# Kernel optimization log

Measured on AMD Instinct MI355X. Metric: run time of the kernel, lower is better.

## Reference

```python
import jax, jax.numpy as jnp
import numpy as np

NG = 1024      # graphs
NPG = 128      # nodes per graph (forced by lin1 = Linear(128*hid, 128))
N = NG * NPG   # 131072 nodes
DEG = 16       # avg in-graph degree
E = N * DEG    # 2,097,152 edges
IN, H = 4, 64


def setup_inputs() -> dict:
    key = jax.random.key(0)
    ks = jax.random.split(key, 24)
    x = jax.random.normal(ks[0], (N, IN), jnp.float32)
    # edges constrained within each 128-node graph
    src = jax.random.randint(ks[1], (E,), 0, NPG)
    dst = jax.random.randint(ks[2], (E,), 0, NPG)
    off = jnp.repeat(jnp.arange(NG, dtype=jnp.int32) * NPG, NPG * DEG)
    edge_index = jnp.stack([src.astype(jnp.int32) + off, dst.astype(jnp.int32) + off])
    g = lambda k, shp, fan: jax.random.normal(k, shp, jnp.float32) / np.float32(np.sqrt(fan))
    return {
        "x": x, "edge_index": edge_index,
        # GATv2Conv(4->64)
        "Wl": g(ks[3], (IN, H), IN), "bl": jnp.zeros((H,), jnp.float32),
        "Wr": g(ks[4], (IN, H), IN), "br": jnp.zeros((H,), jnp.float32),
        "att_v2": g(ks[5], (H,), H), "b_v2": jnp.zeros((H,), jnp.float32),
        # GATConv #1 (64->64)
        "Wg1": g(ks[6], (H, H), H), "as1": g(ks[7], (H,), H),
        "ad1": g(ks[8], (H,), H), "bg1": jnp.zeros((H,), jnp.float32),
        # GATConv #2 (64->64)
        "Wg2": g(ks[9], (H, H), H), "as2": g(ks[10], (H,), H),
        "ad2": g(ks[11], (H,), H), "bg2": jnp.zeros((H,), jnp.float32),
        # LayerNorm(64)
        "ln_g": jnp.ones((H,), jnp.float32), "ln_b": jnp.zeros((H,), jnp.float32),
        # heads: Linear(128*64 -> 128), Linear(128 -> 1)
        "W1": g(ks[12], (NPG * H, 128), NPG * H), "b1": jnp.zeros((128,), jnp.float32),
        "W2": g(ks[13], (128, 1), 128), "b2": jnp.zeros((1,), jnp.float32),
    }


def _seg_softmax(logits, seg):
    # stable softmax over edges grouped by destination node
    m = jax.ops.segment_max(logits, seg, num_segments=N)
    ex = jnp.exp(logits - m[seg])
    s = jax.ops.segment_sum(ex, seg, num_segments=N)
    return ex / (s[seg] + 1e-16)


def _gatv2(x, src, dst, Wl, bl, Wr, br, att, bias):
    xl = x @ Wl + bl                       # source transform [N,H]
    xr = x @ Wr + br                       # target transform [N,H]
    e = jax.nn.leaky_relu(xl[src] + xr[dst], 0.2) @ att   # [E]
    a = _seg_softmax(e, dst)
    out = jax.ops.segment_sum(a[:, None] * xl[src], dst, num_segments=N)
    return out + bias


def _gat(x, src, dst, W, a_src, a_dst, bias):
    # GATConv default: add self-loops
    loop = jnp.arange(N, dtype=src.dtype)
    s2 = jnp.concatenate([src, loop]); d2 = jnp.concatenate([dst, loop])
    xw = x @ W                             # [N,H]
    al_s = xw @ a_src; al_d = xw @ a_dst   # per-node attention halves [N]
    e = jax.nn.leaky_relu(al_s[s2] + al_d[d2], 0.2)
    a = _seg_softmax(e, d2)
    out = jax.ops.segment_sum(a[:, None] * xw[s2], d2, num_segments=N)
    return out + bias


def _layernorm(x, g, b, eps=1e-5):
    mu = jnp.mean(x, -1, keepdims=True)
    var = jnp.mean(jnp.square(x - mu), -1, keepdims=True)
    return (x - mu) * jax.lax.rsqrt(var + eps) * g + b


def reference(x, edge_index, Wl, bl, Wr, br, att_v2, b_v2,
              Wg1, as1, ad1, bg1, Wg2, as2, ad2, bg2,
              ln_g, ln_b, W1, b1, W2, b2):
    src, dst = edge_index[0], edge_index[1]
    h = jax.nn.leaky_relu(_gatv2(x, src, dst, Wl, bl, Wr, br, att_v2, b_v2), 0.01)
    h = _layernorm(h, ln_g, ln_b)
    h = jax.nn.relu(_gat(h, src, dst, Wg1, as1, ad1, bg1))
    h = jax.nn.relu(_gat(h, src, dst, Wg2, as2, ad2, bg2))
    # linearize: batch is sorted with exactly NPG nodes per graph -> reshape
    h = h.reshape(NG, NPG * H)
    h = jax.nn.leaky_relu(h @ W1 + b1, 0.01)
    return jax.nn.sigmoid(h @ W2 + b2)     # [NG, 1]
```

## Files before the change

kernel.cpp:

```cpp
#include <hip/hip_runtime.h>
#include <hip/hip_bf16.h>

#define NGRAPH 1024
#define NPG 128
#define EPG 2048
#define ETOT (NGRAPH*NPG*16)
#define HD 64

typedef unsigned int uint;
typedef unsigned short ushort_t;
typedef __attribute__((ext_vector_type(8))) short s8v;
typedef __attribute__((ext_vector_type(4))) float f32x4;

#define MFMA16 __builtin_amdgcn_mfma_f32_16x16x32_bf16

__device__ __forceinline__ float lrelu(float x, float s){ return fmaxf(x, x*s); }
__device__ __forceinline__ float b2lo(uint u){ return __uint_as_float(u << 16); }
__device__ __forceinline__ float b2hi(uint u){ return __uint_as_float(u & 0xFFFF0000u); }
__device__ __forceinline__ uint pkbf(float a, float b){
  union { __hip_bfloat162 h; uint u; } t;
  t.h = __hip_bfloat162{__float2bfloat16(a), __float2bfloat16(b)};
  return t.u;
}
__device__ __forceinline__ ushort_t bfb(float v){
  union { __hip_bfloat16 h; ushort_t u; } t; t.h = __float2bfloat16(v); return t.u;
}
union U4S8 { uint4 u; s8v s; };
__device__ __forceinline__ s8v bcs8(uint4 u){ U4S8 t; t.u = u; return t.s; }
__device__ __forceinline__ s8v pk8(uint4 x, uint4 y){
  U4S8 t;
  t.u.x = pkbf(__uint_as_float(x.x), __uint_as_float(x.y));
  t.u.y = pkbf(__uint_as_float(x.z), __uint_as_float(x.w));
  t.u.z = pkbf(__uint_as_float(y.x), __uint_as_float(y.y));
  t.u.w = pkbf(__uint_as_float(y.z), __uint_as_float(y.w));
  return t.s;
}
#define DPP_ADD(v, ctrl) ((v) + __int_as_float(__builtin_amdgcn_update_dpp(0, __float_as_int(v), (ctrl), 0xF, 0xF, false)))

__device__ __forceinline__ int oswz(int r, int p){ return (r<<5) | ((((p>>2) ^ (r & 7))<<2) | (p & 3)); }
__device__ __forceinline__ int obase(int r, int oc){ return (r<<5) | (((oc) ^ (r & 7))<<2); }
__device__ __forceinline__ int t64(int r, int p){ return (r<<6) | ((((p>>2) ^ (r & 15))<<2) | (p & 3)); }
__device__ __forceinline__ int t64b(int r, int q){ return (r<<6) | (((q ^ (r & 15))<<2)); }
__device__ __forceinline__ int fP16(int r, int k){ return (r<<7) | (((((k>>2) ^ r) & 31)<<2) | (k & 3)); }
__device__ __forceinline__ int fP16b(int r, int q){ return (r<<7) | ((((q ^ r) & 31))<<2); }

#define O_H   0
#define O_T   4096
#define O_P   8192
#define O_E   10240
#define O_SOF 12288
#define O_ALS 12353
#define O_ALD 12481
#define SM_SZ 12609

__device__ __forceinline__ void aggregate_rounds(
    uint* SM, const ushort_t* soff16, const float* eva, const ushort_t* edsG,
    const float* selfw, const float* biasp, bool dorelu,
    int tid, int wv, int lw, int lq)
{
  float* Pf = (float*)(SM + O_P);
  ushort_t* sH16 = (ushort_t*)(SM + O_H);
  float bj = biasp[16*wv + lw];
  for (int q = 0; q < 8; q++) {
    uint4 z = {0,0,0,0};
    *(uint4*)&SM[O_P + tid*8]     = z;
    *(uint4*)&SM[O_P + tid*8 + 4] = z;
    __syncthreads();
    int p0 = soff16[q*16], p1 = soff16[q*16 + 16];
    for (int p = p0 + tid; p < p1; p += 256) {
      int sd = edsG[p];
      atomicAdd(&Pf[fP16((sd >> 8) - q*16, sd & 127)], eva[p]);
    }
    if (selfw && tid < 16)
      atomicAdd(&Pf[fP16(tid, q*16 + tid)], selfw[q*16 + tid]);
    __syncthreads();
    f32x4 c = {0.f,0.f,0.f,0.f};
    #pragma unroll
    for (int ks = 0; ks < 4; ks++) {
      int kk = ks*32 + lq*8;
      uint4 f0 = *(uint4*)&Pf[fP16b(lw, (kk>>2))];
      uint4 f1 = *(uint4*)&Pf[fP16b(lw, (kk>>2)+1)];
      s8v a = pk8(f0, f1);
      s8v b = bcs8(*(uint4*)&SM[O_T + t64b(16*wv + lw, kk>>3)]);
      c = MFMA16(a, b, c, 0, 0, 0);
    }
    int col = 16*wv + lw;
    #pragma unroll
    for (int rg = 0; rg < 4; rg++) {
      float v = c[rg] + bj;
      v = dorelu ? fmaxf(v, 0.f) : lrelu(v, 0.01f);
      int r = q*16 + lq*4 + rg;
      sH16[oswz(r, col>>1)*2 + (col&1)] = bfb(v);
    }
    __syncthreads();
  }
}

__global__ __launch_bounds__(256, 3) void gnn_fused(
    const float* __restrict__ x, const int* __restrict__ ei,
    const float* __restrict__ Wl, const float* __restrict__ bl,
    const float* __restrict__ Wr, const float* __restrict__ br,
    const float* __restrict__ att, const float* __restrict__ bv2,
    const float* __restrict__ Wg1, const float* __restrict__ as1,
    const float* __restrict__ ad1, const float* __restrict__ bg1,
    const float* __restrict__ Wg2, const float* __restrict__ as2,
    const float* __restrict__ ad2, const float* __restrict__ bg2,
    const float* __restrict__ lng, const float* __restrict__ lnb,
    uint* __restrict__ hout, uint* __restrict__ edsd_ws)
{
  __shared__ uint SM[SM_SZ];
  float*    eva   = (float*)(SM + O_E);
  ushort_t* soff16= (ushort_t*)(SM + O_SOF);
  float*    als   = (float*)(SM + O_ALS);
  float*    ald   = (float*)(SM + O_ALD);
  ushort_t* sH16  = (ushort_t*)(SM + O_H);
  ushort_t* sT16  = (ushort_t*)(SM + O_T);

  const int g    = blockIdx.x;
  const int tid  = threadIdx.x;
  const int lane = tid & 63;
  const int wv   = tid >> 6;
  const int lw   = lane & 15;
  const int lq   = lane >> 4;
  const int oc   = lane & 7;
  const int ebase = g * EPG;
  uint* eg = edsd_ws + (size_t)g * 1024;
  const ushort_t* edsG = (const ushort_t*)eg;

  {
    int* spos = (int*)(SM + O_P + 1024);
    ushort_t* edsL = (ushort_t*)(SM + O_P);
    if (tid < NPG) spos[tid] = 0;
    __syncthreads();
    for (int e = tid; e < EPG; e += 256)
      atomicAdd(&spos[ei[ETOT + ebase + e] - g*NPG], 1);
    __syncthreads();
    if (wv == 0) {
      int c0 = spos[lane], c1 = spos[lane + 64];
      #pragma unroll
      for (int o = 1; o < 64; o <<= 1) { int t = __shfl_up(c0, o); if (lane >= o) c0 += t; }
      #pragma unroll
      for (int o = 1; o < 64; o <<= 1) { int t = __shfl_up(c1, o); if (lane >= o) c1 += t; }
      int tot0 = __shfl(c0, 63);
      soff16[lane + 1]  = (ushort_t)c0;
      soff16[lane + 65] = (ushort_t)(c1 + tot0);
      if (lane == 0) soff16[0] = 0;
    }
    __syncthreads();
    if (tid < NPG) spos[tid] = soff16[tid];
    __syncthreads();
    for (int e = tid; e < EPG; e += 256) {
      int s = ei[ebase + e] - g*NPG;
      int d = ei[ETOT + ebase + e] - g*NPG;
      int p = atomicAdd(&spos[d], 1);
      edsL[p] = (ushort_t)(s | (d << 8));
    }
    __syncthreads();
  }

  {
    #pragma unroll
    for (int i = 0; i < 4; i++) eg[tid + i*256] = SM[O_P + tid + i*256];

    const int pl = lane & 31, hb = lane >> 5;
    const float2 wl0 = *(const float2*)&Wl[0*64 + 2*pl];
    const float2 wl1 = *(const float2*)&Wl[1*64 + 2*pl];
    const float2 wl2 = *(const float2*)&Wl[2*64 + 2*pl];
    const float2 wl3 = *(const float2*)&Wl[3*64 + 2*pl];
    const float2 wr0 = *(const float2*)&Wr[0*64 + 2*pl];
    const float2 wr1 = *(const float2*)&Wr[1*64 + 2*pl];
    const float2 wr2 = *(const float2*)&Wr[2*64 + 2*pl];
    const float2 wr3 = *(const float2*)&Wr[3*64 + 2*pl];
    const float2 blp = *(const float2*)&bl[2*pl];
    const float2 brp = *(const float2*)&br[2*pl];
    const float4* x4 = (const float4*)x + (size_t)g * NPG;
    for (int st = 0; st < 16; st++) {
      int i = st*8 + wv*2 + hb;
      float4 xi = x4[i];
      float l0 = blp.x + xi.x*wl0.x + xi.y*wl1.x + xi.z*wl2.x + xi.w*wl3.x;
      float l1 = blp.y + xi.x*wl0.y + xi.y*wl1.y + xi.z*wl2.y + xi.w*wl3.y;
      float r0 = brp.x + xi.x*wr0.x + xi.y*wr1.x + xi.z*wr2.x + xi.w*wr3.x;
      float r1 = brp.y + xi.x*wr0.y + xi.y*wr1.y + xi.z*wr2.y + xi.w*wr3.y;
      SM[O_H + oswz(i, pl)] = pkbf(l0, l1);
      SM[O_T + oswz(i, pl)] = pkbf(r0, r1);
    }
  }
  __syncthreads();

  {
    const int grp = lane >> 3;
    const ushort_t* edsL = (const ushort_t*)(SM + O_P);
    float4 atA = *(const float4*)&att[oc*8];
    float4 atB = *(const float4*)&att[oc*8 + 4];
    int base = wv * 512;
    for (int stp = 0; stp < 64; stp++) {
      int e  = base + stp*8 + grp;
      int sd = edsL[e];
      int s  = sd & 127, d = sd >> 8;
      uint4 ql = *(uint4*)&SM[O_H + obase(s, oc)];
      uint4 qr = *(uint4*)&SM[O_T + obase(d, oc)];
      float acc, v;
      v = b2lo(ql.x)+b2lo(qr.x); acc  = lrelu(v,0.2f)*atA.x;
      v = b2hi(ql.x)+b2hi(qr.x); acc += lrelu(v,0.2f)*atA.y;
      v = b2lo(ql.y)+b2lo(qr.y); acc += lrelu(v,0.2f)*atA.z;
      v = b2hi(ql.y)+b2hi(qr.y); acc += lrelu(v,0.2f)*atA.w;
      v = b2lo(ql.z)+b2lo(qr.z); acc += lrelu(v,0.2f)*atB.x;
      v = b2hi(ql.z)+b2hi(qr.z); acc += lrelu(v,0.2f)*atB.y;
      v = b2lo(ql.w)+b2lo(qr.w); acc += lrelu(v,0.2f)*atB.z;
      v = b2hi(ql.w)+b2hi(qr.w); acc += lrelu(v,0.2f)*atB.w;
      acc = DPP_ADD(acc, 0x111); acc = DPP_ADD(acc, 0x112); acc = DPP_ADD(acc, 0x114);
      if ((lane & 7) == 7) eva[e] = acc;
    }
  }
  __syncthreads();

  {
    const int g16 = tid >> 4, sl = tid & 15;
    for (int it = 0; it < 8; it++) {
      int d = it*16 + g16;
      int p0 = soff16[d], p1 = soff16[d+1];
      float m = -1e30f;
      for (int p = p0 + sl; p < p1; p += 16) m = fmaxf(m, eva[p]);
      #pragma unroll
      for (int o = 1; o < 16; o <<= 1) m = fmaxf(m, __shfl_xor(m, o));
      float ssum = 0.f;
      for (int p = p0 + sl; p < p1; p += 16) { float ex = __expf(eva[p]-m); ssum += ex; eva[p] = ex; }
      #pragma unroll
      for (int o = 1; o < 16; o <<= 1) ssum += __shfl_xor(ssum, o);
      float rnm = 1.f / (ssum + 1e-16f);
      for (int p = p0 + sl; p < p1; p += 16) eva[p] *= rnm;
    }
    ushort_t* xl16 = (ushort_t*)(SM + O_H);
    int j = tid & 63, spb = tid >> 6;
    for (int i = 0; i < 16; i++) {
      int sp = spb*16 + i;
      float v0 = __uint_as_float((uint)xl16[oswz(2*sp,   j>>1)*2 + (j&1)] << 16);
      float v1 = __uint_as_float((uint)xl16[oswz(2*sp+1, j>>1)*2 + (j&1)] << 16);
      SM[O_T + t64(j, sp)] = pkbf(v0, v1);
    }
  }
  __syncthreads();

  aggregate_rounds(SM, soff16, eva, edsG, nullptr, bv2, false, tid, wv, lw, lq);

  {
    int pl = lane & 31, hb = lane >> 5;
    float2 gv = *(const float2*)&lng[2*pl];
    float2 bv = *(const float2*)&lnb[2*pl];
    for (int it = 0; it < 16; it++) {
      int d = it*8 + wv*2 + hb;
      uint w = SM[O_H + oswz(d, pl)];
      float v0 = b2lo(w), v1 = b2hi(w);
      float s1 = v0 + v1, s2 = v0*v0 + v1*v1;
      #pragma unroll
      for (int o = 1; o < 32; o <<= 1) { s1 += __shfl_xor(s1, o); s2 += __shfl_xor(s2, o); }
      float mu  = s1 * 0.015625f;
      float var = s2 * 0.015625f - mu*mu;
      float rs  = rsqrtf(var + 1e-5f);
      SM[O_H + oswz(d, pl)] = pkbf((v0-mu)*rs*gv.x + bv.x, (v1-mu)*rs*gv.y + bv.y);
    }
  }
  __syncthreads();

  for (int layer = 0; layer < 2; layer++) {
    const float* Wg  = layer ? Wg2 : Wg1;
    const float* avs = layer ? as2 : as1;
    const float* avd = layer ? ad2 : ad1;
    const float* bg  = layer ? bg2 : bg1;
    float* was = (float*)(SM + O_P);
    float* wad = was + 64;
    ushort_t* wg16 = (ushort_t*)(SM + O_E);

    if (tid < 128) {
      const float* av = (tid < 64) ? avs : avd;
      float* dst = (tid < 64) ? was : wad;
      int k = tid & 63;
      float acc = 0.f;
      #pragma unroll
      for (int jj = 0; jj < 16; jj++) {
        float4 w = *(const float4*)&Wg[k*64 + jj*4];
        float4 a = *(const float4*)&av[jj*4];
        acc += w.x*a.x + w.y*a.y + w.z*a.z + w.w*a.w;
      }
      dst[k] = acc;
    } else {
      int t2 = tid - 128;
      #pragma unroll
      for (int i = 0; i < 8; i++) {
        int idx = t2 + i*128;
        int k = idx >> 4, j4 = (idx & 15)*4;
        float4 w = *(const float4*)&Wg[k*64 + j4];
        wg16[oswz(j4+0, k>>1)*2 + (k&1)] = bfb(w.x);
        wg16[oswz(j4+1, k>>1)*2 + (k&1)] = bfb(w.y);
        wg16[oswz(j4+2, k>>1)*2 + (k&1)] = bfb(w.z);
        wg16[oswz(j4+3, k>>1)*2 + (k&1)] = bfb(w.w);
      }
    }
    __syncthreads();

    {
      int row = 16*wv + lw;
      s8v a0 = bcs8(*(uint4*)&SM[O_E + obase(row, lq)]);
      s8v a1 = bcs8(*(uint4*)&SM[O_E + obase(row, 4+lq)]);
      #pragma unroll
      for (int nt = 0; nt < 8; nt++) {
        int d = nt*16 + lw;
        s8v b0 = bcs8(*(uint4*)&SM[O_H + obase(d, lq)]);
        s8v b1 = bcs8(*(uint4*)&SM[O_H + obase(d, 4+lq)]);
        f32x4 c = {0.f,0.f,0.f,0.f};
        c = MFMA16(a0, b0, c, 0, 0, 0);
        c = MFMA16(a1, b1, c, 0, 0, 0);
        int j0 = 16*wv + lq*4;
        #pragma unroll
        for (int rg = 0; rg < 4; rg++)
          sT16[t64(j0+rg, d>>1)*2 + (d&1)] = bfb(c[rg]);
      }
    }
    __syncthreads();

    {
      float4 ws0 = *(float4*)&was[oc*8], ws1 = *(float4*)&was[oc*8 + 4];
      float4 wd0 = *(float4*)&wad[oc*8], wd1 = *(float4*)&wad[oc*8 + 4];
      for (int ps = 0; ps < 4; ps++) {
        int n = ps*32 + (tid >> 3);
        uint4 q = *(uint4*)&SM[O_H + obase(n, oc)];
        float f0=b2lo(q.x), f1=b2hi(q.x), f2=b2lo(q.y), f3=b2hi(q.y);
        float f4=b2lo(q.z), f5=b2hi(q.z), f6=b2lo(q.w), f7=b2hi(q.w);
        float sa = f0*ws0.x+f1*ws0.y+f2*ws0.z+f3*ws0.w+f4*ws1.x+f5*ws1.y+f6*ws1.z+f7*ws1.w;
        float sd = f0*wd0.x+f1*wd0.y+f2*wd0.z+f3*wd0.w+f4*wd1.x+f5*wd1.y+f6*wd1.z+f7*wd1.w;
        sa = DPP_ADD(sa, 0x111); sa = DPP_ADD(sa, 0x112); sa = DPP_ADD(sa, 0x114);
        sd = DPP_ADD(sd, 0x111); sd = DPP_ADD(sd, 0x112); sd = DPP_ADD(sd, 0x114);
        if ((lane & 7) == 7) { als[n] = sa; ald[n] = sd; }
      }
    }
    __syncthreads();

    #pragma unroll
    for (int i = 0; i < 4; i++) {
      uint w = eg[tid + i*256];
      int e = (tid + i*256)*2;
      int sd0 = w & 0xFFFF, sd1 = w >> 16;
      eva[e]   = lrelu(als[sd0 & 127] + ald[sd0 >> 8], 0.2f);
      eva[e+1] = lrelu(als[sd1 & 127] + ald[sd1 >> 8], 0.2f);
    }
    __syncthreads();

    {
      const int g16 = tid >> 4, sl = tid & 15;
      for (int it = 0; it < 8; it++) {
        int d = it*16 + g16;
        int p0 = soff16[d], p1 = soff16[d+1];
        float se = lrelu(als[d] + ald[d], 0.2f);
        float m = se;
        for (int p = p0 + sl; p < p1; p += 16) m = fmaxf(m, eva[p]);
        #pragma unroll
        for (int o = 1; o < 16; o <<= 1) m = fmaxf(m, __shfl_xor(m, o));
        float ex0 = __expf(se - m);
        float ssum = 0.f;
        for (int p = p0 + sl; p < p1; p += 16) { float ex = __expf(eva[p]-m); ssum += ex; eva[p] = ex; }
        #pragma unroll
        for (int o = 1; o < 16; o <<= 1) ssum += __shfl_xor(ssum, o);
        float rnm = 1.f / (ssum + ex0 + 1e-16f);
        for (int p = p0 + sl; p < p1; p += 16) eva[p] *= rnm;
        if (sl == 0) als[d] = ex0 * rnm;
      }
    }
    __syncthreads();

    aggregate_rounds(SM, soff16, eva, edsG, als, bg, true, tid, wv, lw, lq);
  }

  {
    uint* hg = hout + (size_t)g * 4096;
    #pragma unroll
    for (int i = 0; i < 16; i++) {
      int idx = tid + i*256;
      hg[idx] = SM[O_H + oswz(idx >> 5, idx & 31)];
    }
  }
}

__global__ __launch_bounds__(256) void w1_transpose(const float* __restrict__ W1,
                                                    uint* __restrict__ w1t)
{
  __shared__ float sw[64*130];
  const int tid = threadIdx.x;
  const int k0 = blockIdx.x * 64;
  #pragma unroll
  for (int i = 0; i < 8; i++) {
    int idx = tid + i*256;
    int r = idx >> 5, c4 = (idx & 31)*4;
    *(float4*)&sw[r*130 + c4] = *(const float4*)&W1[(size_t)(k0+r)*128 + c4];
  }
  __syncthreads();
  #pragma unroll
  for (int i = 0; i < 16; i++) {
    int idx = tid + i*256;
    int c = idx >> 5, kp = idx & 31;
    w1t[(size_t)c*4096 + (k0>>1) + kp] = pkbf(sw[(2*kp)*130 + c], sw[(2*kp+1)*130 + c]);
  }
}

__global__ __launch_bounds__(256) void head_gemm(
    const uint* __restrict__ hbuf, const uint* __restrict__ w1t,
    float* __restrict__ partial)
{
  __shared__ uint sAh[2048];
  __shared__ uint sBh[4096];
  const int tid = threadIdx.x, lane = tid & 63, wv = tid >> 6;
  const int lw = lane & 15, lq = lane >> 4;
  const int g0 = blockIdx.x * 64;
  const int ks = blockIdx.y;
  f32x4 acc[8];
  #pragma unroll
  for (int i = 0; i < 8; i++) acc[i] = f32x4{0.f,0.f,0.f,0.f};

  for (int ch = 0; ch < 8; ch++) {
    int pb = ks*256 + ch*32;
    #pragma unroll
    for (int i = 0; i < 2; i++) {
      int idx = tid + i*256; int r = idx >> 3, q4 = idx & 7;
      uint4 v = *(const uint4*)&hbuf[(size_t)(g0+r)*4096 + pb + q4*4];
      *(uint4*)&sAh[(r<<5) | ((q4 ^ (r & 7))<<2)] = v;
    }
    #pragma unroll
    for (int i = 0; i < 4; i++) {
      int idx = tid + i*256; int r = idx >> 3, q4 = idx & 7;
      uint4 v = *(const uint4*)&w1t[(size_t)r*4096 + pb + q4*4];
      *(uint4*)&sBh[(r<<5) | ((q4 ^ (r & 7))<<2)] = v;
    }
    __syncthreads();
    int ra = 16*wv + lw;
    s8v a0 = bcs8(*(uint4*)&sAh[obase(ra, lq)]);
    s8v a1 = bcs8(*(uint4*)&sAh[obase(ra, 4+lq)]);
    #pragma unroll
    for (int nt = 0; nt < 8; nt++) {
      int c = nt*16 + lw;
      s8v b0 = bcs8(*(uint4*)&sBh[obase(c, lq)]);
      s8v b1 = bcs8(*(uint4*)&sBh[obase(c, 4+lq)]);
      acc[nt] = MFMA16(a0, b0, acc[nt], 0, 0, 0);
      acc[nt] = MFMA16(a1, b1, acc[nt], 0, 0, 0);
    }
    __syncthreads();
  }
  float* pp = partial + (size_t)ks*131072;
  #pragma unroll
  for (int nt = 0; nt < 8; nt++) {
    int c = nt*16 + lw;
    int r0 = g0 + 16*wv + lq*4;
    #pragma unroll
    for (int rg = 0; rg < 4; rg++)
      pp[(size_t)(r0+rg)*128 + c] = acc[nt][rg];
  }
}

__global__ __launch_bounds__(64) void head_out(
    const float* __restrict__ partial, const float* __restrict__ b1,
    const float* __restrict__ W2, const float* __restrict__ b2,
    float* __restrict__ out)
{
  const int g = blockIdx.x;
  const int l = threadIdx.x;
  float v0 = b1[l], v1 = b1[64 + l];
  #pragma unroll
  for (int s = 0; s < 16; s++) {
    v0 += partial[(size_t)s*131072 + g*128 + l];
    v1 += partial[(size_t)s*131072 + g*128 + 64 + l];
  }
  float sum = lrelu(v0, 0.01f)*W2[l] + lrelu(v1, 0.01f)*W2[64 + l];
  #pragma unroll
  for (int m = 32; m > 0; m >>= 1) sum += __shfl_xor(sum, m);
  if (l == 0) out[g] = 1.f / (1.f + __expf(-(sum + b2[0])));
}

extern "C" void kernel_launch(void* const* d_in, const int* in_sizes, int n_in,
                              void* d_out, int out_size, void* d_ws, size_t ws_size,
                              hipStream_t stream) {
  const float* x   = (const float*)d_in[0];
  const int*   ei  = (const int*)  d_in[1];
  const float* Wl  = (const float*)d_in[2];
  const float* bl_ = (const float*)d_in[3];
  const float* Wr  = (const float*)d_in[4];
  const float* br_ = (const float*)d_in[5];
  const float* att = (const float*)d_in[6];
  const float* bv2 = (const float*)d_in[7];
  const float* Wg1 = (const float*)d_in[8];
  const float* as1 = (const float*)d_in[9];
  const float* ad1 = (const float*)d_in[10];
  const float* bg1 = (const float*)d_in[11];
  const float* Wg2 = (const float*)d_in[12];
  const float* as2 = (const float*)d_in[13];
  const float* ad2 = (const float*)d_in[14];
  const float* bg2 = (const float*)d_in[15];
  const float* lng = (const float*)d_in[16];
  const float* lnb = (const float*)d_in[17];
  const float* W1  = (const float*)d_in[18];
  const float* b1  = (const float*)d_in[19];
  const float* W2  = (const float*)d_in[20];
  const float* b2  = (const float*)d_in[21];
  float* out = (float*)d_out;

  uint*  hbuf    = (uint*)d_ws;
  float* partial = (float*)((char*)d_ws + (size_t)16*1024*1024);
  uint*  w1t     = (uint*)((char*)d_ws + (size_t)24*1024*1024);
  uint*  edsd_ws = (uint*)((char*)d_ws + (size_t)26*1024*1024);

  w1_transpose<<<128, 256, 0, stream>>>(W1, w1t);
  gnn_fused<<<NGRAPH, 256, 0, stream>>>(x, ei, Wl, bl_, Wr, br_, att, bv2,
      Wg1, as1, ad1, bg1, Wg2, as2, ad2, bg2, lng, lnb, hbuf, edsd_ws);
  head_gemm<<<dim3(16, 16), 256, 0, stream>>>(hbuf, w1t, partial);
  head_out<<<NGRAPH, 64, 0, stream>>>(partial, b1, W2, b2, out);
}
```

Measured before the change: 309.4 us.

## Replace dense MFMA aggregation with per-destination CSR gather softmax-aggregate

Drops the dense 128x128 attention-matrix build (LDS atomics, then MFMA against a transposed feature tile) in all three GAT layers. Each destination node is now handled by an 8-lane group that walks its CSR edge list, computes the logits, does the segment softmax and accumulates the weighted source features directly, using online prefetch of the next edge. This also removes the global edge-list scratch round-trip and several block barriers and transpose passes. The head_out kernel is retiled to 8 graphs per 256-thread block with float4 loads. The cost is serialized per-edge loops with uneven degree per lane group and repeated exp evaluations in place of tensor-core matmuls.

```diff
diff --git a/kernel.cpp b/kernel.cpp
--- a/kernel.cpp
+++ b/kernel.cpp
@@ -5,7 +5,6 @@
 #define NPG 128
 #define EPG 2048
 #define ETOT (NGRAPH*NPG*16)
-#define HD 64
 
 typedef unsigned int uint;
 typedef unsigned short ushort_t;
@@ -27,74 +26,27 @@
 }
 union U4S8 { uint4 u; s8v s; };
 __device__ __forceinline__ s8v bcs8(uint4 u){ U4S8 t; t.u = u; return t.s; }
-__device__ __forceinline__ s8v pk8(uint4 x, uint4 y){
-  U4S8 t;
-  t.u.x = pkbf(__uint_as_float(x.x), __uint_as_float(x.y));
-  t.u.y = pkbf(__uint_as_float(x.z), __uint_as_float(x.w));
-  t.u.z = pkbf(__uint_as_float(y.x), __uint_as_float(y.y));
-  t.u.w = pkbf(__uint_as_float(y.z), __uint_as_float(y.w));
-  return t.s;
-}
 #define DPP_ADD(v, ctrl) ((v) + __int_as_float(__builtin_amdgcn_update_dpp(0, __float_as_int(v), (ctrl), 0xF, 0xF, false)))
 
 __device__ __forceinline__ int oswz(int r, int p){ return (r<<5) | ((((p>>2) ^ (r & 7))<<2) | (p & 3)); }
 __device__ __forceinline__ int obase(int r, int oc){ return (r<<5) | (((oc) ^ (r & 7))<<2); }
-__device__ __forceinline__ int t64(int r, int p){ return (r<<6) | ((((p>>2) ^ (r & 15))<<2) | (p & 3)); }
-__device__ __forceinline__ int t64b(int r, int q){ return (r<<6) | (((q ^ (r & 15))<<2)); }
-__device__ __forceinline__ int fP16(int r, int k){ return (r<<7) | (((((k>>2) ^ r) & 31)<<2) | (k & 3)); }
-__device__ __forceinline__ int fP16b(int r, int q){ return (r<<7) | ((((q ^ r) & 31))<<2); }
-
-#define O_H   0
-#define O_T   4096
-#define O_P   8192
-#define O_E   10240
-#define O_SOF 12288
-#define O_ALS 12353
-#define O_ALD 12481
-#define SM_SZ 12609
-
-__device__ __forceinline__ void aggregate_rounds(
-    uint* SM, const ushort_t* soff16, const float* eva, const ushort_t* edsG,
-    const float* selfw, const float* biasp, bool dorelu,
-    int tid, int wv, int lw, int lq)
-{
-  float* Pf = (float*)(SM + O_P);
-  ushort_t* sH16 = (ushort_t*)(SM + O_H);
-  float bj = biasp[16*wv + lw];
-  for (int q = 0; q < 8; q++) {
-    uint4 z = {0,0,0,0};
-    *(uint4*)&SM[O_P + tid*8]     = z;
-    *(uint4*)&SM[O_P + tid*8 + 4] = z;
-    __syncthreads();
-    int p0 = soff16[q*16], p1 = soff16[q*16 + 16];
-    for (int p = p0 + tid; p < p1; p += 256) {
-      int sd = edsG[p];
-      atomicAdd(&Pf[fP16((sd >> 8) - q*16, sd & 127)], eva[p]);
-    }
-    if (selfw && tid < 16)
-      atomicAdd(&Pf[fP16(tid, q*16 + tid)], selfw[q*16 + tid]);
-    __syncthreads();
-    f32x4 c = {0.f,0.f,0.f,0.f};
-    #pragma unroll
-    for (int ks = 0; ks < 4; ks++) {
-      int kk = ks*32 + lq*8;
-      uint4 f0 = *(uint4*)&Pf[fP16b(lw, (kk>>2))];
-      uint4 f1 = *(uint4*)&Pf[fP16b(lw, (kk>>2)+1)];
-      s8v a = pk8(f0, f1);
-      s8v b = bcs8(*(uint4*)&SM[O_T + t64b(16*wv + lw, kk>>3)]);
-      c = MFMA16(a, b, c, 0, 0, 0);
-    }
-    int col = 16*wv + lw;
-    #pragma unroll
-    for (int rg = 0; rg < 4; rg++) {
-      float v = c[rg] + bj;
-      v = dorelu ? fmaxf(v, 0.f) : lrelu(v, 0.01f);
-      int r = q*16 + lq*4 + rg;
-      sH16[oswz(r, col>>1)*2 + (col&1)] = bfb(v);
-    }
-    __syncthreads();
-  }
-}
+
+__device__ __forceinline__ void fma8(float* acc, uint4 q, float a){
+  acc[0] += a*b2lo(q.x); acc[1] += a*b2hi(q.x);
+  acc[2] += a*b2lo(q.y); acc[3] += a*b2hi(q.y);
+  acc[4] += a*b2lo(q.z); acc[5] += a*b2hi(q.z);
+  acc[6] += a*b2lo(q.w); acc[7] += a*b2hi(q.w);
+}
+
+#define O_A   0
+#define O_B   4096
+#define O_EVA 8192
+#define O_ED  10240
+#define O_WS  11264
+#define O_SOF 11392
+#define O_ALS 11457
+#define O_ALD 11585
+#define SM_SZ 11713
 
 __global__ __launch_bounds__(256, 3) void gnn_fused(
     const float* __restrict__ x, const int* __restrict__ ei,
@@ -106,15 +58,18 @@
     const float* __restrict__ Wg2, const float* __restrict__ as2,
     const float* __restrict__ ad2, const float* __restrict__ bg2,
     const float* __restrict__ lng, const float* __restrict__ lnb,
-    uint* __restrict__ hout, uint* __restrict__ edsd_ws)
+    uint* __restrict__ hout)
 {
   __shared__ uint SM[SM_SZ];
-  float*    eva   = (float*)(SM + O_E);
-  ushort_t* soff16= (ushort_t*)(SM + O_SOF);
-  float*    als   = (float*)(SM + O_ALS);
-  float*    ald   = (float*)(SM + O_ALD);
-  ushort_t* sH16  = (ushort_t*)(SM + O_H);
-  ushort_t* sT16  = (ushort_t*)(SM + O_T);
+  float*    eva    = (float*)(SM + O_EVA);
+  ushort_t* edsL   = (ushort_t*)(SM + O_ED);
+  ushort_t* soff16 = (ushort_t*)(SM + O_SOF);
+  float*    als    = (float*)(SM + O_ALS);
+  float*    ald    = (float*)(SM + O_ALD);
+  float*    was    = (float*)(SM + O_WS);
+  float*    wad    = was + 64;
+  ushort_t* wgA16  = (ushort_t*)(SM + O_A);
+  ushort_t* wg16   = (ushort_t*)(SM + O_EVA);
 
   const int g    = blockIdx.x;
   const int tid  = threadIdx.x;
@@ -122,14 +77,12 @@
   const int wv   = tid >> 6;
   const int lw   = lane & 15;
   const int lq   = lane >> 4;
-  const int oc   = lane & 7;
+  const int sl   = lane & 7;
+  const int grp  = lane >> 3;
   const int ebase = g * EPG;
-  uint* eg = edsd_ws + (size_t)g * 1024;
-  const ushort_t* edsG = (const ushort_t*)eg;
 
   {
-    int* spos = (int*)(SM + O_P + 1024);
-    ushort_t* edsL = (ushort_t*)(SM + O_P);
+    int* spos = (int*)(SM + O_EVA);
     if (tid < NPG) spos[tid] = 0;
     __syncthreads();
     for (int e = tid; e < EPG; e += 256)
@@ -155,13 +108,9 @@
       int p = atomicAdd(&spos[d], 1);
       edsL[p] = (ushort_t)(s | (d << 8));
     }
-    __syncthreads();
   }
 
   {
-    #pragma unroll
-    for (int i = 0; i < 4; i++) eg[tid + i*256] = SM[O_P + tid + i*256];
-
     const int pl = lane & 31, hb = lane >> 5;
     const float2 wl0 = *(const float2*)&Wl[0*64 + 2*pl];
     const float2 wl1 = *(const float2*)&Wl[1*64 + 2*pl];
@@ -181,67 +130,70 @@
       float l1 = blp.y + xi.x*wl0.y + xi.y*wl1.y + xi.z*wl2.y + xi.w*wl3.y;
       float r0 = brp.x + xi.x*wr0.x + xi.y*wr1.x + xi.z*wr2.x + xi.w*wr3.x;
       float r1 = brp.y + xi.x*wr0.y + xi.y*wr1.y + xi.z*wr2.y + xi.w*wr3.y;
-      SM[O_H + oswz(i, pl)] = pkbf(l0, l1);
-      SM[O_T + oswz(i, pl)] = pkbf(r0, r1);
+      SM[O_A + oswz(i, pl)] = pkbf(l0, l1);
+      SM[O_B + oswz(i, pl)] = pkbf(r0, r1);
     }
   }
   __syncthreads();
 
   {
-    const int grp = lane >> 3;
-    const ushort_t* edsL = (const ushort_t*)(SM + O_P);
-    float4 atA = *(const float4*)&att[oc*8];
-    float4 atB = *(const float4*)&att[oc*8 + 4];
-    int base = wv * 512;
-    for (int stp = 0; stp < 64; stp++) {
-      int e  = base + stp*8 + grp;
-      int sd = edsL[e];
-      int s  = sd & 127, d = sd >> 8;
-      uint4 ql = *(uint4*)&SM[O_H + obase(s, oc)];
-      uint4 qr = *(uint4*)&SM[O_T + obase(d, oc)];
-      float acc, v;
-      v = b2lo(ql.x)+b2lo(qr.x); acc  = lrelu(v,0.2f)*atA.x;
-      v = b2hi(ql.x)+b2hi(qr.x); acc += lrelu(v,0.2f)*atA.y;
-      v = b2lo(ql.y)+b2lo(qr.y); acc += lrelu(v,0.2f)*atA.z;
-      v = b2hi(ql.y)+b2hi(qr.y); acc += lrelu(v,0.2f)*atA.w;
-      v = b2lo(ql.z)+b2lo(qr.z); acc += lrelu(v,0.2f)*atB.x;
-      v = b2hi(ql.z)+b2hi(qr.z); acc += lrelu(v,0.2f)*atB.y;
-      v = b2lo(ql.w)+b2lo(qr.w); acc += lrelu(v,0.2f)*atB.z;
-      v = b2hi(ql.w)+b2hi(qr.w); acc += lrelu(v,0.2f)*atB.w;
-      acc = DPP_ADD(acc, 0x111); acc = DPP_ADD(acc, 0x112); acc = DPP_ADD(acc, 0x114);
-      if ((lane & 7) == 7) eva[e] = acc;
+    float4 atA = *(const float4*)&att[sl*8];
+    float4 atB = *(const float4*)&att[sl*8 + 4];
+    float4 bvA = *(const float4*)&bv2[sl*8];
+    float4 bvB = *(const float4*)&bv2[sl*8 + 4];
+    for (int pass = 0; pass < 4; pass++) {
+      int d  = wv*32 + pass*8 + grp;
+      int p0 = soff16[d], p1 = soff16[d+1];
+      uint4 qr = *(uint4*)&SM[O_B + obase(d, sl)];
+      float m = -1e30f;
+      if (p0 < p1) {
+        int sN = edsL[p0] & 127;
+        uint4 qN = *(uint4*)&SM[O_A + obase(sN, sl)];
+        for (int e = p0; e < p1; e++) {
+          uint4 ql = qN;
+          if (e + 1 < p1) { sN = edsL[e+1] & 127; qN = *(uint4*)&SM[O_A + obase(sN, sl)]; }
+          float pt;
+          pt  = lrelu(b2lo(ql.x)+b2lo(qr.x), 0.2f)*atA.x;
+          pt += lrelu(b2hi(ql.x)+b2hi(qr.x), 0.2f)*atA.y;
+          pt += lrelu(b2lo(ql.y)+b2lo(qr.y), 0.2f)*atA.z;
+          pt += lrelu(b2hi(ql.y)+b2hi(qr.y), 0.2f)*atA.w;
+          pt += lrelu(b2lo(ql.z)+b2lo(qr.z), 0.2f)*atB.x;
+          pt += lrelu(b2hi(ql.z)+b2hi(qr.z), 0.2f)*atB.y;
+          pt += lrelu(b2lo(ql.w)+b2lo(qr.w), 0.2f)*atB.z;
+          pt += lrelu(b2hi(ql.w)+b2hi(qr.w), 0.2f)*atB.w;
+          pt += __shfl_xor(pt, 1); pt += __shfl_xor(pt, 2); pt += __shfl_xor(pt, 4);
+          if (sl == 0) eva[e] = pt;
+          m = fmaxf(m, pt);
+        }
+      }
+      float ss = 0.f;
+      for (int e = p0 + sl; e < p1; e += 8) ss += __expf(eva[e] - m);
+      ss += __shfl_xor(ss, 1); ss += __shfl_xor(ss, 2); ss += __shfl_xor(ss, 4);
+      float rnm = 1.f / (ss + 1e-16f);
+      float acc[8] = {0,0,0,0,0,0,0,0};
+      if (p0 < p1) {
+        int sN = edsL[p0] & 127;
+        uint4 qN = *(uint4*)&SM[O_A + obase(sN, sl)];
+        float evN = eva[p0];
+        for (int e = p0; e < p1; e++) {
+          uint4 ql = qN; float ev = evN;
+          if (e + 1 < p1) {
+            sN = edsL[e+1] & 127;
+            qN = *(uint4*)&SM[O_A + obase(sN, sl)];
+            evN = eva[e+1];
+          }
+          fma8(acc, ql, __expf(ev - m) * rnm);
+        }
+      }
+      uint4 o;
+      o.x = pkbf(lrelu(acc[0]+bvA.x,0.01f), lrelu(acc[1]+bvA.y,0.01f));
+      o.y = pkbf(lrelu(acc[2]+bvA.z,0.01f), lrelu(acc[3]+bvA.w,0.01f));
+      o.z = pkbf(lrelu(acc[4]+bvB.x,0.01f), lrelu(acc[5]+bvB.y,0.01f));
+      o.w = pkbf(lrelu(acc[6]+bvB.z,0.01f), lrelu(acc[7]+bvB.w,0.01f));
+      *(uint4*)&SM[O_B + obase(d, sl)] = o;
     }
   }
   __syncthreads();
-
-  {
-    const int g16 = tid >> 4, sl = tid & 15;
-    for (int it = 0; it < 8; it++) {
-      int d = it*16 + g16;
-      int p0 = soff16[d], p1 = soff16[d+1];
-      float m = -1e30f;
-      for (int p = p0 + sl; p < p1; p += 16) m = fmaxf(m, eva[p]);
-      #pragma unroll
-      for (int o = 1; o < 16; o <<= 1) m = fmaxf(m, __shfl_xor(m, o));
-      float ssum = 0.f;
-      for (int p = p0 + sl; p < p1; p += 16) { float ex = __expf(eva[p]-m); ssum += ex; eva[p] = ex; }
-      #pragma unroll
-      for (int o = 1; o < 16; o <<= 1) ssum += __shfl_xor(ssum, o);
-      float rnm = 1.f / (ssum + 1e-16f);
-      for (int p = p0 + sl; p < p1; p += 16) eva[p] *= rnm;
-    }
-    ushort_t* xl16 = (ushort_t*)(SM + O_H);
-    int j = tid & 63, spb = tid >> 6;
-    for (int i = 0; i < 16; i++) {
-      int sp = spb*16 + i;
-      float v0 = __uint_as_float((uint)xl16[oswz(2*sp,   j>>1)*2 + (j&1)] << 16);
-      float v1 = __uint_as_float((uint)xl16[oswz(2*sp+1, j>>1)*2 + (j&1)] << 16);
-      SM[O_T + t64(j, sp)] = pkbf(v0, v1);
-    }
-  }
-  __syncthreads();
-
-  aggregate_rounds(SM, soff16, eva, edsG, nullptr, bv2, false, tid, wv, lw, lq);
 
   {
     int pl = lane & 31, hb = lane >> 5;
@@ -249,7 +201,7 @@
     float2 bv = *(const float2*)&lnb[2*pl];
     for (int it = 0; it < 16; it++) {
       int d = it*8 + wv*2 + hb;
-      uint w = SM[O_H + oswz(d, pl)];
+      uint w = SM[O_B + oswz(d, pl)];
       float v0 = b2lo(w), v1 = b2hi(w);
       float s1 = v0 + v1, s2 = v0*v0 + v1*v1;
       #pragma unroll
@@ -257,7 +209,7 @@
       float mu  = s1 * 0.015625f;
       float var = s2 * 0.015625f - mu*mu;
       float rs  = rsqrtf(var + 1e-5f);
-      SM[O_H + oswz(d, pl)] = pkbf((v0-mu)*rs*gv.x + bv.x, (v1-mu)*rs*gv.y + bv.y);
+      SM[O_B + oswz(d, pl)] = pkbf((v0-mu)*rs*gv.x + bv.x, (v1-mu)*rs*gv.y + bv.y);
     }
   }
   __syncthreads();
@@ -267,9 +219,6 @@
     const float* avs = layer ? as2 : as1;
     const float* avd = layer ? ad2 : ad1;
     const float* bg  = layer ? bg2 : bg1;
-    float* was = (float*)(SM + O_P);
-    float* wad = was + 64;
-    ushort_t* wg16 = (ushort_t*)(SM + O_E);
 
     if (tid < 128) {
       const float* av = (tid < 64) ? avs : avd;
@@ -300,30 +249,28 @@
 
     {
       int row = 16*wv + lw;
-      s8v a0 = bcs8(*(uint4*)&SM[O_E + obase(row, lq)]);
-      s8v a1 = bcs8(*(uint4*)&SM[O_E + obase(row, 4+lq)]);
+      s8v a0 = bcs8(*(uint4*)&SM[O_EVA + obase(row, lq)]);
+      s8v a1 = bcs8(*(uint4*)&SM[O_EVA + obase(row, 4+lq)]);
+      int j0 = 16*wv + lq*4;
       #pragma unroll
       for (int nt = 0; nt < 8; nt++) {
         int d = nt*16 + lw;
-        s8v b0 = bcs8(*(uint4*)&SM[O_H + obase(d, lq)]);
-        s8v b1 = bcs8(*(uint4*)&SM[O_H + obase(d, 4+lq)]);
+        s8v b0 = bcs8(*(uint4*)&SM[O_B + obase(d, lq)]);
+        s8v b1 = bcs8(*(uint4*)&SM[O_B + obase(d, 4+lq)]);
         f32x4 c = {0.f,0.f,0.f,0.f};
         c = MFMA16(a0, b0, c, 0, 0, 0);
         c = MFMA16(a1, b1, c, 0, 0, 0);
-        int j0 = 16*wv + lq*4;
         #pragma unroll
-        for (int rg = 0; rg < 4; rg++)
-          sT16[t64(j0+rg, d>>1)*2 + (d&1)] = bfb(c[rg]);
-      }
-    }
-    __syncthreads();
-
-    {
-      float4 ws0 = *(float4*)&was[oc*8], ws1 = *(float4*)&was[oc*8 + 4];
-      float4 wd0 = *(float4*)&wad[oc*8], wd1 = *(float4*)&wad[oc*8 + 4];
+        for (int rg = 0; rg < 4; rg++) {
+          int j = j0 + rg;
+          wgA16[oswz(d, j>>1)*2 + (j&1)] = bfb(c[rg]);
+        }
+      }
+      float4 ws0 = *(float4*)&was[sl*8], ws1 = *(float4*)&was[sl*8 + 4];
+      float4 wd0 = *(float4*)&wad[sl*8], wd1 = *(float4*)&wad[sl*8 + 4];
       for (int ps = 0; ps < 4; ps++) {
         int n = ps*32 + (tid >> 3);
-        uint4 q = *(uint4*)&SM[O_H + obase(n, oc)];
+        uint4 q = *(uint4*)&SM[O_B + obase(n, sl)];
         float f0=b2lo(q.x), f1=b2hi(q.x), f2=b2lo(q.y), f3=b2hi(q.y);
         float f4=b2lo(q.z), f5=b2hi(q.z), f6=b2lo(q.w), f7=b2hi(q.w);
         float sa = f0*ws0.x+f1*ws0.y+f2*ws0.z+f3*ws0.w+f4*ws1.x+f5*ws1.y+f6*ws1.z+f7*ws1.w;
@@ -335,39 +282,49 @@
     }
     __syncthreads();
 
-    #pragma unroll
-    for (int i = 0; i < 4; i++) {
-      uint w = eg[tid + i*256];
-      int e = (tid + i*256)*2;
-      int sd0 = w & 0xFFFF, sd1 = w >> 16;
-      eva[e]   = lrelu(als[sd0 & 127] + ald[sd0 >> 8], 0.2f);
-      eva[e+1] = lrelu(als[sd1 & 127] + ald[sd1 >> 8], 0.2f);
-    }
-    __syncthreads();
-
     {
-      const int g16 = tid >> 4, sl = tid & 15;
-      for (int it = 0; it < 8; it++) {
-        int d = it*16 + g16;
+      float4 bgA = *(const float4*)&bg[sl*8];
+      float4 bgB = *(const float4*)&bg[sl*8 + 4];
+      for (int pass = 0; pass < 4; pass++) {
+        int d  = wv*32 + pass*8 + grp;
         int p0 = soff16[d], p1 = soff16[d+1];
-        float se = lrelu(als[d] + ald[d], 0.2f);
-        float m = se;
-        for (int p = p0 + sl; p < p1; p += 16) m = fmaxf(m, eva[p]);
-        #pragma unroll
-        for (int o = 1; o < 16; o <<= 1) m = fmaxf(m, __shfl_xor(m, o));
-        float ex0 = __expf(se - m);
-        float ssum = 0.f;
-        for (int p = p0 + sl; p < p1; p += 16) { float ex = __expf(eva[p]-m); ssum += ex; eva[p] = ex; }
-        #pragma unroll
-        for (int o = 1; o < 16; o <<= 1) ssum += __shfl_xor(ssum, o);
-        float rnm = 1.f / (ssum + ex0 + 1e-16f);
-        for (int p = p0 + sl; p < p1; p += 16) eva[p] *= rnm;
-        if (sl == 0) als[d] = ex0 * rnm;
-      }
-    }
-    __syncthreads();
-
-    aggregate_rounds(SM, soff16, eva, edsG, als, bg, true, tid, wv, lw, lq);
+        float ald_d = ald[d];
+        float lgs = lrelu(als[d] + ald_d, 0.2f);
+        float m = lgs;
+        for (int e = p0 + sl; e < p1; e += 8)
+          m = fmaxf(m, lrelu(als[edsL[e] & 127] + ald_d, 0.2f));
+        m = fmaxf(m, __shfl_xor(m, 1)); m = fmaxf(m, __shfl_xor(m, 2)); m = fmaxf(m, __shfl_xor(m, 4));
+        float ex0 = __expf(lgs - m);
+        float ss = (sl == 0) ? ex0 : 0.f;
+        for (int e = p0 + sl; e < p1; e += 8)
+          ss += __expf(lrelu(als[edsL[e] & 127] + ald_d, 0.2f) - m);
+        ss += __shfl_xor(ss, 1); ss += __shfl_xor(ss, 2); ss += __shfl_xor(ss, 4);
+        float rnm = 1.f / (ss + 1e-16f);
+        float acc[8] = {0,0,0,0,0,0,0,0};
+        fma8(acc, *(uint4*)&SM[O_A + obase(d, sl)], ex0 * rnm);
+        if (p0 < p1) {
+          int sN = edsL[p0] & 127;
+          float alN = als[sN];
+          uint4 qN = *(uint4*)&SM[O_A + obase(sN, sl)];
+          for (int e = p0; e < p1; e++) {
+            uint4 ql = qN; float alv = alN;
+            if (e + 1 < p1) {
+              sN = edsL[e+1] & 127;
+              alN = als[sN];
+              qN = *(uint4*)&SM[O_A + obase(sN, sl)];
+            }
+            fma8(acc, ql, __expf(lrelu(alv + ald_d, 0.2f) - m) * rnm);
+          }
+        }
+        uint4 o;
+        o.x = pkbf(fmaxf(acc[0]+bgA.x,0.f), fmaxf(acc[1]+bgA.y,0.f));
+        o.y = pkbf(fmaxf(acc[2]+bgA.z,0.f), fmaxf(acc[3]+bgA.w,0.f));
+        o.z = pkbf(fmaxf(acc[4]+bgB.x,0.f), fmaxf(acc[5]+bgB.y,0.f));
+        o.w = pkbf(fmaxf(acc[6]+bgB.z,0.f), fmaxf(acc[7]+bgB.w,0.f));
+        *(uint4*)&SM[O_B + obase(d, sl)] = o;
+      }
+    }
+    __syncthreads();
   }
 
   {
@@ -375,7 +332,7 @@
     #pragma unroll
     for (int i = 0; i < 16; i++) {
       int idx = tid + i*256;
-      hg[idx] = SM[O_H + oswz(idx >> 5, idx & 31)];
+      hg[idx] = SM[O_B + oswz(idx >> 5, idx & 31)];
     }
   }
 }
@@ -454,23 +411,27 @@
   }
 }
 
-__global__ __launch_bounds__(64) void head_out(
+__global__ __launch_bounds__(256) void head_out(
     const float* __restrict__ partial, const float* __restrict__ b1,
     const float* __restrict__ W2, const float* __restrict__ b2,
     float* __restrict__ out)
 {
-  const int g = blockIdx.x;
-  const int l = threadIdx.x;
-  float v0 = b1[l], v1 = b1[64 + l];
+  const int tid = threadIdx.x;
+  const int gl  = tid >> 5;
+  const int c4  = tid & 31;
+  const int g   = blockIdx.x*8 + gl;
+  float4 v = *(const float4*)&b1[c4*4];
   #pragma unroll
   for (int s = 0; s < 16; s++) {
-    v0 += partial[(size_t)s*131072 + g*128 + l];
-    v1 += partial[(size_t)s*131072 + g*128 + 64 + l];
-  }
-  float sum = lrelu(v0, 0.01f)*W2[l] + lrelu(v1, 0.01f)*W2[64 + l];
-  #pragma unroll
-  for (int m = 32; m > 0; m >>= 1) sum += __shfl_xor(sum, m);
-  if (l == 0) out[g] = 1.f / (1.f + __expf(-(sum + b2[0])));
+    float4 p = *(const float4*)&partial[(size_t)s*131072 + (size_t)g*128 + c4*4];
+    v.x += p.x; v.y += p.y; v.z += p.z; v.w += p.w;
+  }
+  float4 w = *(const float4*)&W2[c4*4];
+  float t = lrelu(v.x,0.01f)*w.x + lrelu(v.y,0.01f)*w.y
+          + lrelu(v.z,0.01f)*w.z + lrelu(v.w,0.01f)*w.w;
+  #pragma unroll
+  for (int m = 1; m < 32; m <<= 1) t += __shfl_xor(t, m);
+  if (c4 == 0) out[g] = 1.f / (1.f + __expf(-(t + b2[0])));
 }
 
 extern "C" void kernel_launch(void* const* d_in, const int* in_sizes, int n_in,
@@ -503,11 +464,10 @@
   uint*  hbuf    = (uint*)d_ws;
   float* partial = (float*)((char*)d_ws + (size_t)16*1024*1024);
   uint*  w1t     = (uint*)((char*)d_ws + (size_t)24*1024*1024);
-  uint*  edsd_ws = (uint*)((char*)d_ws + (size_t)26*1024*1024);
 
   w1_transpose<<<128, 256, 0, stream>>>(W1, w1t);
   gnn_fused<<<NGRAPH, 256, 0, stream>>>(x, ei, Wl, bl_, Wr, br_, att, bv2,
-      Wg1, as1, ad1, bg1, Wg2, as2, ad2, bg2, lng, lnb, hbuf, edsd_ws);
+      Wg1, as1, ad1, bg1, Wg2, as2, ad2, bg2, lng, lnb, hbuf);
   head_gemm<<<dim3(16, 16), 256, 0, stream>>>(hbuf, w1t, partial);
-  head_out<<<NGRAPH, 64, 0, stream>>>(partial, b1, W2, b2, out);
-}
+  head_out<<<128, 256, 0, stream>>>(partial, b1, W2, b2, out);
+}
```

After: 314.7 us. Within noise of the previous version (+1.7%).
